# Optimization experiments

Measured on AMD Instinct MI355X. Metric: run time of the kernel, lower is better.

The kernel has to match this reference:

```python
import jax, jax.numpy as jnp
import numpy as np

B, NQ, NK, H = 4, 256, 512, 256

def setup_inputs() -> dict:
    key = jax.random.key(0)
    k1, k2, k3, k4, k5 = jax.random.split(key, 5)
    s = 1.0 / np.sqrt(H)
    return {
        "x_query": jax.random.normal(k1, (B, NQ, H), dtype=jnp.float32),
        "x_key": jax.random.normal(k2, (B, NK, H), dtype=jnp.float32),
        "w1": jax.random.uniform(k3, (H, H), jnp.float32, -s, s),  # torch Linear weight (out,in)
        "w2": jax.random.uniform(k4, (H, H), jnp.float32, -s, s),
        "v": jax.random.uniform(k5, (1, H), jnp.float32, -s, s),
    }

def reference(x_query, x_key, w1, w2, v):
    # key_transform: (B, NK, H); query_transform: (B, NQ, H)
    kt = jnp.einsum('bkh,oh->bko', x_key, w1)
    qt = jnp.einsum('bqh,oh->bqo', x_query, w2)
    # broadcast add -> (B, NQ, NK, H), tanh, project with v -> (B, NQ, NK)
    prod = jnp.einsum('bqkh,h->bqk', jnp.tanh(kt[:, None, :, :] + qt[:, :, None, :]), v[0])
    return jax.nn.log_softmax(prod, axis=-1)
```

## Files before the change

kernel.cpp:

```cpp
#include <hip/hip_runtime.h>

#define B_  4
#define NQ_ 256
#define NK_ 512
#define H_  256
#define PADE 516

#define TWO_LOG2E 2.8853900817779268f

__global__ __launch_bounds__(256)
void gemm_fused(const float* __restrict__ xq, const float* __restrict__ xk,
                const float* __restrict__ w1, const float* __restrict__ w2,
                float* __restrict__ Ebuf,
                float* __restrict__ Fbuf)
{
    constexpr int BK = 32;
    const float* A; const float* Bm;
    int m0, n0, bz; bool iskt;
    {
        int id = blockIdx.x;
        if (id < 128) {
            iskt = true;
            bz = id >> 5; int t = id & 31;
            m0 = (t >> 3) * 64; n0 = (t & 7) * 64;
            A = w1; Bm = xk + (long)bz * NK_ * H_;
        } else {
            iskt = false;
            id -= 128;
            bz = id >> 4; int t = id & 15;
            m0 = (t >> 2) * 64; n0 = (t & 3) * 64;
            A = xq + (long)bz * NQ_ * H_; Bm = w2;
        }
    }
    const int lda = H_, ldb = H_;

    __shared__ float As[BK][68];
    __shared__ float Bs[BK][68];

    const int tid  = threadIdx.x;
    const int lrow = tid >> 2;
    const int lk   = (tid & 3) * 8;
    const int tm   = (tid >> 4) * 4;
    const int tn   = (tid & 15) * 4;

    float acc[4][4] = {};

    float4 a0_r = *(const float4*)&A [(long)(m0 + lrow) * lda + lk];
    float4 a1_r = *(const float4*)&A [(long)(m0 + lrow) * lda + lk + 4];
    float4 b0_r = *(const float4*)&Bm[(long)(n0 + lrow) * ldb + lk];
    float4 b1_r = *(const float4*)&Bm[(long)(n0 + lrow) * ldb + lk + 4];
    float4 a0_n = a0_r, a1_n = a1_r, b0_n = b0_r, b1_n = b1_r;

    for (int kt = 0; kt < H_; kt += BK) {
        __syncthreads();
        As[lk+0][lrow]=a0_r.x; As[lk+1][lrow]=a0_r.y; As[lk+2][lrow]=a0_r.z; As[lk+3][lrow]=a0_r.w;
        As[lk+4][lrow]=a1_r.x; As[lk+5][lrow]=a1_r.y; As[lk+6][lrow]=a1_r.z; As[lk+7][lrow]=a1_r.w;
        Bs[lk+0][lrow]=b0_r.x; Bs[lk+1][lrow]=b0_r.y; Bs[lk+2][lrow]=b0_r.z; Bs[lk+3][lrow]=b0_r.w;
        Bs[lk+4][lrow]=b1_r.x; Bs[lk+5][lrow]=b1_r.y; Bs[lk+6][lrow]=b1_r.z; Bs[lk+7][lrow]=b1_r.w;
        if (kt + BK < H_) {
            a0_n = *(const float4*)&A [(long)(m0 + lrow) * lda + kt + BK + lk];
            a1_n = *(const float4*)&A [(long)(m0 + lrow) * lda + kt + BK + lk + 4];
            b0_n = *(const float4*)&Bm[(long)(n0 + lrow) * ldb + kt + BK + lk];
            b1_n = *(const float4*)&Bm[(long)(n0 + lrow) * ldb + kt + BK + lk + 4];
        }
        __syncthreads();
        #pragma unroll
        for (int kk = 0; kk < BK; ++kk) {
            float4 av = *(const float4*)&As[kk][tm];
            float4 bv = *(const float4*)&Bs[kk][tn];
            float am[4] = {av.x, av.y, av.z, av.w};
            float bn[4] = {bv.x, bv.y, bv.z, bv.w};
            #pragma unroll
            for (int i = 0; i < 4; ++i)
                #pragma unroll
                for (int j = 0; j < 4; ++j)
                    acc[i][j] = fmaf(am[i], bn[j], acc[i][j]);
        }
        a0_r = a0_n; a1_r = a1_n; b0_r = b0_n; b1_r = b1_n;
    }

    if (iskt) {
        float4* cb = (float4*)Ebuf + ((long)bz * 64 + ((m0 + tm) >> 2)) * PADE;
        #pragma unroll
        for (int j = 0; j < 4; ++j) {
            float4 e4 = { __builtin_amdgcn_exp2f(acc[0][j] * TWO_LOG2E),
                          __builtin_amdgcn_exp2f(acc[1][j] * TWO_LOG2E),
                          __builtin_amdgcn_exp2f(acc[2][j] * TWO_LOG2E),
                          __builtin_amdgcn_exp2f(acc[3][j] * TWO_LOG2E) };
            cb[n0 + tn + j] = e4;
        }
    } else {
        #pragma unroll
        for (int i = 0; i < 4; ++i) {
            float4 f4v = { __builtin_amdgcn_exp2f(acc[i][0] * TWO_LOG2E),
                           __builtin_amdgcn_exp2f(acc[i][1] * TWO_LOG2E),
                           __builtin_amdgcn_exp2f(acc[i][2] * TWO_LOG2E),
                           __builtin_amdgcn_exp2f(acc[i][3] * TWO_LOG2E) };
            *(float4*)&Fbuf[((long)bz * NQ_ + m0 + tm + i) * H_ + n0 + tn] = f4v;
        }
    }
}

__global__ __launch_bounds__(512, 2)
void attn_main(const float4* __restrict__ E4,
               const float* __restrict__ Fbuf,
               const float* __restrict__ v,
               float* __restrict__ out)
{
    const int k = threadIdx.x, b = blockIdx.y, q0 = blockIdx.x * 2;

    const float4* kp  = E4 + (long)b * 64 * PADE + k;
    const float4* F0p = (const float4*)(Fbuf + ((long)b * NQ_ + q0) * H_);
    const float4* F1p = F0p + (H_ / 4);
    const float4* v4p = (const float4*)v;

    float T0 = 0.f, T1 = 0.f;

    float4 ka0 = kp[0*PADE], ka1 = kp[1*PADE], ka2 = kp[2*PADE], ka3 = kp[3*PADE];
    float4 kb0 = kp[4*PADE], kb1 = kp[5*PADE], kb2 = kp[6*PADE], kb3 = kp[7*PADE];
    float4 kc0 = ka0, kc1 = ka1, kc2 = ka2, kc3 = ka3;

#define PROC4(EV, HC)                                                         \
    {                                                                         \
        float4 f0 = F0p[HC];                   \
        float4 f1 = F1p[HC];                                                  \
        float4 vv = v4p[HC];                                                  \
        {                                                             \
            float d0 = fmaf(EV.x, f0.x, 1.f), d1 = fmaf(EV.y, f0.y, 1.f);     \
            float d2 = fmaf(EV.z, f0.z, 1.f), d3 = fmaf(EV.w, f0.w, 1.f);     \
            float D01 = d0 * d1, D23 = d2 * d3;                               \
            float N01 = fmaf(vv.x, d1, vv.y * d0);                            \
            float N23 = fmaf(vv.z, d3, vv.w * d2);                            \
            float N   = fmaf(N01, D23, N23 * D01);                            \
            T0 = fmaf(N, __builtin_amdgcn_rcpf(D01 * D23), T0);               \
        }                                                                     \
        {                                                             \
            float d0 = fmaf(EV.x, f1.x, 1.f), d1 = fmaf(EV.y, f1.y, 1.f);     \
            float d2 = fmaf(EV.z, f1.z, 1.f), d3 = fmaf(EV.w, f1.w, 1.f);     \
            float D01 = d0 * d1, D23 = d2 * d3;                               \
            float N01 = fmaf(vv.x, d1, vv.y * d0);                            \
            float N23 = fmaf(vv.z, d3, vv.w * d2);                            \
            float N   = fmaf(N01, D23, N23 * D01);                            \
            T1 = fmaf(N, __builtin_amdgcn_rcpf(D01 * D23), T1);               \
        }                                                                     \
    }

    for (int g = 0; g < 64; g += 4) {
        if (g + 8 < 64) {
            kc0 = kp[(long)(g +  8) * PADE];
            kc1 = kp[(long)(g +  9) * PADE];
            kc2 = kp[(long)(g + 10) * PADE];
            kc3 = kp[(long)(g + 11) * PADE];
        }
        PROC4(ka0, g + 0)
        PROC4(ka1, g + 1)
        PROC4(ka2, g + 2)
        PROC4(ka3, g + 3)
        ka0 = kb0; ka1 = kb1; ka2 = kb2; ka3 = kb3;
        kb0 = kc0; kb1 = kc1; kb2 = kc2; kb3 = kc3;
    }
#undef PROC4

    float val0 = -2.f * T0;
    float val1 = -2.f * T1;

    __shared__ float red[8][2];
    const int lane = k & 63, wv = k >> 6;

    float e0 = __builtin_amdgcn_exp2f(val0 * 1.4426950408889634f);
    float e1 = __builtin_amdgcn_exp2f(val1 * 1.4426950408889634f);
    #pragma unroll
    for (int o = 32; o; o >>= 1) {
        e0 += __shfl_xor(e0, o, 64);
        e1 += __shfl_xor(e1, o, 64);
    }
    if (lane == 0) { red[wv][0] = e0; red[wv][1] = e1; }
    __syncthreads();
    float s0 = 0.f, s1 = 0.f;
    #pragma unroll
    for (int w = 0; w < 8; ++w) { s0 += red[w][0]; s1 += red[w][1]; }

    float l0 = __builtin_amdgcn_logf(s0) * 0.6931471805599453f;
    float l1 = __builtin_amdgcn_logf(s1) * 0.6931471805599453f;
    out[((long)b * NQ_ + q0 + 0) * NK_ + k] = val0 - l0;
    out[((long)b * NQ_ + q0 + 1) * NK_ + k] = val1 - l1;
}

extern "C" void kernel_launch(void* const* d_in, const int* in_sizes, int n_in,
                              void* d_out, int out_size, void* d_ws, size_t ws_size,
                              hipStream_t stream)
{
    const float* xq = (const float*)d_in[0];
    const float* xk = (const float*)d_in[1];
    const float* w1 = (const float*)d_in[2];
    const float* w2 = (const float*)d_in[3];
    const float* v  = (const float*)d_in[4];
    float* out = (float*)d_out;

    float* Ebuf = (float*)d_ws;
    float* Fbuf = Ebuf + (size_t)B_ * 64 * PADE * 4;

    gemm_fused<<<dim3(192), 256, 0, stream>>>(xq, xk, w1, w2, Ebuf, Fbuf);
    attn_main<<<dim3(NQ_ / 2, B_), 512, 0, stream>>>(
        (const float4*)Ebuf, Fbuf, v, out);
}
```

Measured before the change: 38.24 us.

## Store key exponentials as fp16 in 8-wide interleaved layout

The key-side exp(2*kt) buffer is now stored as fp16, clamped to 60000, in a layout that packs 8 hidden channels per key so each thread loads one 16-byte half8 per 8 channels instead of a float4 per 4. This halves the bytes the attention kernel streams per key and the number of load instructions, at the cost of fp16 conversions in the inner loop. Reduced precision and the clamp on large exponentials may shift the tanh values slightly. The prefetch depth also changes from two groups ahead to one.

```diff
diff --git a/kernel.cpp b/kernel.cpp
--- a/kernel.cpp
+++ b/kernel.cpp
@@ -4,14 +4,17 @@
 #define NQ_ 256
 #define NK_ 512
 #define H_  256
-#define PADE 516
+#define PADK 520
+
+typedef _Float16 half8  __attribute__((ext_vector_type(8)));
+typedef _Float16 half4_t __attribute__((ext_vector_type(4)));
 
 #define TWO_LOG2E 2.8853900817779268f
 
 __global__ __launch_bounds__(256)
 void gemm_fused(const float* __restrict__ xq, const float* __restrict__ xk,
                 const float* __restrict__ w1, const float* __restrict__ w2,
-                float* __restrict__ Ebuf,
+                _Float16* __restrict__ Ebuf,
                 float* __restrict__ Fbuf)
 {
     constexpr int BK = 32;
@@ -80,14 +83,16 @@
     }
 
     if (iskt) {
-        float4* cb = (float4*)Ebuf + ((long)bz * 64 + ((m0 + tm) >> 2)) * PADE;
+        const long gbase = ((long)bz * 32 + ((m0 + tm) >> 3)) * PADK * 8 + (tm & 7);
         #pragma unroll
         for (int j = 0; j < 4; ++j) {
-            float4 e4 = { __builtin_amdgcn_exp2f(acc[0][j] * TWO_LOG2E),
-                          __builtin_amdgcn_exp2f(acc[1][j] * TWO_LOG2E),
-                          __builtin_amdgcn_exp2f(acc[2][j] * TWO_LOG2E),
-                          __builtin_amdgcn_exp2f(acc[3][j] * TWO_LOG2E) };
-            cb[n0 + tn + j] = e4;
+            half4_t h4;
+            #pragma unroll
+            for (int i = 0; i < 4; ++i) {
+                float e = __builtin_amdgcn_exp2f(acc[i][j] * TWO_LOG2E);
+                h4[i] = (_Float16)fminf(e, 60000.0f);
+            }
+            *(half4_t*)&Ebuf[gbase + (long)(n0 + tn + j) * 8] = h4;
         }
     } else {
         #pragma unroll
@@ -102,64 +107,62 @@
 }
 
 __global__ __launch_bounds__(512, 2)
-void attn_main(const float4* __restrict__ E4,
+void attn_main(const half8* __restrict__ Eh,
                const float* __restrict__ Fbuf,
                const float* __restrict__ v,
                float* __restrict__ out)
 {
     const int k = threadIdx.x, b = blockIdx.y, q0 = blockIdx.x * 2;
 
-    const float4* kp  = E4 + (long)b * 64 * PADE + k;
+    const half8* kp   = Eh + (long)b * 32 * PADK + k;
     const float4* F0p = (const float4*)(Fbuf + ((long)b * NQ_ + q0) * H_);
     const float4* F1p = F0p + (H_ / 4);
     const float4* v4p = (const float4*)v;
 
     float T0 = 0.f, T1 = 0.f;
 
-    float4 ka0 = kp[0*PADE], ka1 = kp[1*PADE], ka2 = kp[2*PADE], ka3 = kp[3*PADE];
-    float4 kb0 = kp[4*PADE], kb1 = kp[5*PADE], kb2 = kp[6*PADE], kb3 = kp[7*PADE];
-    float4 kc0 = ka0, kc1 = ka1, kc2 = ka2, kc3 = ka3;
-
-#define PROC4(EV, HC)                                                         \
+    half8 ka0 = kp[0*PADK], ka1 = kp[1*PADK], ka2 = kp[2*PADK], ka3 = kp[3*PADK];
+    half8 kn0 = ka0, kn1 = ka1, kn2 = ka2, kn3 = ka3;
+
+#define QTERM(T, E0, E1, E2, E3, FQ, VV)                                      \
     {                                                                         \
-        float4 f0 = F0p[HC];                   \
-        float4 f1 = F1p[HC];                                                  \
-        float4 vv = v4p[HC];                                                  \
-        {                                                             \
-            float d0 = fmaf(EV.x, f0.x, 1.f), d1 = fmaf(EV.y, f0.y, 1.f);     \
-            float d2 = fmaf(EV.z, f0.z, 1.f), d3 = fmaf(EV.w, f0.w, 1.f);     \
-            float D01 = d0 * d1, D23 = d2 * d3;                               \
-            float N01 = fmaf(vv.x, d1, vv.y * d0);                            \
-            float N23 = fmaf(vv.z, d3, vv.w * d2);                            \
-            float N   = fmaf(N01, D23, N23 * D01);                            \
-            T0 = fmaf(N, __builtin_amdgcn_rcpf(D01 * D23), T0);               \
-        }                                                                     \
-        {                                                             \
-            float d0 = fmaf(EV.x, f1.x, 1.f), d1 = fmaf(EV.y, f1.y, 1.f);     \
-            float d2 = fmaf(EV.z, f1.z, 1.f), d3 = fmaf(EV.w, f1.w, 1.f);     \
-            float D01 = d0 * d1, D23 = d2 * d3;                               \
-            float N01 = fmaf(vv.x, d1, vv.y * d0);                            \
-            float N23 = fmaf(vv.z, d3, vv.w * d2);                            \
-            float N   = fmaf(N01, D23, N23 * D01);                            \
-            T1 = fmaf(N, __builtin_amdgcn_rcpf(D01 * D23), T1);               \
-        }                                                                     \
-    }
-
-    for (int g = 0; g < 64; g += 4) {
-        if (g + 8 < 64) {
-            kc0 = kp[(long)(g +  8) * PADE];
-            kc1 = kp[(long)(g +  9) * PADE];
-            kc2 = kp[(long)(g + 10) * PADE];
-            kc3 = kp[(long)(g + 11) * PADE];
-        }
-        PROC4(ka0, g + 0)
-        PROC4(ka1, g + 1)
-        PROC4(ka2, g + 2)
-        PROC4(ka3, g + 3)
-        ka0 = kb0; ka1 = kb1; ka2 = kb2; ka3 = kb3;
-        kb0 = kc0; kb1 = kc1; kb2 = kc2; kb3 = kc3;
-    }
-#undef PROC4
+        float d0 = fmaf(E0, FQ.x, 1.f), d1 = fmaf(E1, FQ.y, 1.f);             \
+        float d2 = fmaf(E2, FQ.z, 1.f), d3 = fmaf(E3, FQ.w, 1.f);             \
+        float D01 = d0 * d1, D23 = d2 * d3;                                   \
+        float N01 = fmaf(VV.x, d1, VV.y * d0);                                \
+        float N23 = fmaf(VV.z, d3, VV.w * d2);                                \
+        float N   = fmaf(N01, D23, N23 * D01);                                \
+        T = fmaf(N, __builtin_amdgcn_rcpf(D01 * D23), T);                     \
+    }
+#define PROW(KV, R)                                                           \
+    {                                                                         \
+        float e0 = (float)KV[0], e1 = (float)KV[1], e2 = (float)KV[2],        \
+              e3 = (float)KV[3], e4 = (float)KV[4], e5 = (float)KV[5],        \
+              e6 = (float)KV[6], e7 = (float)KV[7];                           \
+        float4 va  = v4p[2*(R)],   vb  = v4p[2*(R)+1];                        \
+        float4 f0a = F0p[2*(R)],   f0b = F0p[2*(R)+1];                        \
+        float4 f1a = F1p[2*(R)],   f1b = F1p[2*(R)+1];                        \
+        QTERM(T0, e0, e1, e2, e3, f0a, va)                                    \
+        QTERM(T0, e4, e5, e6, e7, f0b, vb)                                    \
+        QTERM(T1, e0, e1, e2, e3, f1a, va)                                    \
+        QTERM(T1, e4, e5, e6, e7, f1b, vb)                                    \
+    }
+
+    for (int g = 0; g < 32; g += 4) {
+        if (g + 4 < 32) {
+            kn0 = kp[(long)(g + 4) * PADK];
+            kn1 = kp[(long)(g + 5) * PADK];
+            kn2 = kp[(long)(g + 6) * PADK];
+            kn3 = kp[(long)(g + 7) * PADK];
+        }
+        PROW(ka0, g + 0)
+        PROW(ka1, g + 1)
+        PROW(ka2, g + 2)
+        PROW(ka3, g + 3)
+        ka0 = kn0; ka1 = kn1; ka2 = kn2; ka3 = kn3;
+    }
+#undef PROW
+#undef QTERM
 
     float val0 = -2.f * T0;
     float val1 = -2.f * T1;
@@ -197,10 +200,10 @@
     const float* v  = (const float*)d_in[4];
     float* out = (float*)d_out;
 
-    float* Ebuf = (float*)d_ws;
-    float* Fbuf = Ebuf + (size_t)B_ * 64 * PADE * 4;
+    _Float16* Ebuf = (_Float16*)d_ws;
+    float* Fbuf = (float*)((char*)d_ws + (size_t)B_ * 32 * PADK * 8 * 2);
 
     gemm_fused<<<dim3(192), 256, 0, stream>>>(xq, xk, w1, w2, Ebuf, Fbuf);
     attn_main<<<dim3(NQ_ / 2, B_), 512, 0, stream>>>(
-        (const float4*)Ebuf, Fbuf, v, out);
+        (const half8*)Ebuf, Fbuf, v, out);
 }
```

Result: faster. 35.37 us (-7.5%).
